# Kernel optimization log

Hardware: AMD Instinct MI355X
Metric: run time of the kernel (lower is better)

Reference implementation:

```python
import jax, jax.numpy as jnp
import numpy as np

B, D, C, K = 1024, 64, 100000, 5  # batch, feature dim, n_classes, positives per sample


def setup_inputs() -> dict:
    key = jax.random.key(0)
    k1, k2, k3 = jax.random.split(key, 3)
    x = jax.random.normal(k1, (B, D), dtype=jnp.float32)
    W = jax.random.normal(k2, (D, C), dtype=jnp.float32) * 0.02
    b = jnp.zeros((C,), dtype=jnp.float32)
    # K distinct positive class ids per sample (setdiff1d assume_unique requires distinct)
    base = jax.random.randint(k3, (B, 1), 0, C)
    labels = (base + jnp.arange(K, dtype=jnp.int64)[None, :]) % C
    return {"x": x, "labels": labels, "W": W, "b": b}


def reference(x, labels, W, b):
    # classifier: logits [B, C]
    logits = x @ W + b
    # Original loop: for each positive p of a sample, CE over [p] + negatives
    # (negatives = all classes except ALL positives of that sample), label 0:
    #   loss_p = -(l_p - log(exp(l_p) + sum_{c in negatives} exp(l_c)))
    # Vectorized via total expsum minus the positives' contribution.
    m = jnp.max(logits, axis=1, keepdims=True)                    # [B, 1]
    e = jnp.exp(logits - m)                                       # [B, C]
    total = jnp.sum(e, axis=1, keepdims=True)                     # [B, 1]
    pos_logits = jnp.take_along_axis(logits, labels, axis=1)      # [B, K]
    pos_e = jnp.exp(pos_logits - m)                               # [B, K]
    neg_sum = total - jnp.sum(pos_e, axis=1, keepdims=True)       # [B, 1]
    denom = pos_e + neg_sum                                       # [B, K]
    losses = -(pos_logits - m - jnp.log(denom))                   # [B, K]
    # sum over all (sample, positive) pairs / total number of positives
    return jnp.sum(losses) / losses.size
```

## Files before the change

### kernel.cpp

```cpp
#include <hip/hip_runtime.h>

constexpr int Bn = 1024;
constexpr int Dn = 64;
constexpr int Cn = 100000;
constexpr int Kn = 5;
constexpr float LOG2E = 1.44269504088896f;
constexpr float LN2   = 0.69314718055994531f;

typedef float f32x4  __attribute__((ext_vector_type(4)));
typedef short bf16x8 __attribute__((ext_vector_type(8)));

__device__ __forceinline__ unsigned short f32_to_bf16(float f) {
  union { float f; unsigned int u; } v; v.f = f;
  unsigned int r = v.u + 0x7FFFu + ((v.u >> 16) & 1u);
  return (unsigned short)(r >> 16);
}
__device__ __forceinline__ float bf16_to_f32(unsigned short u) {
  union { unsigned int i; float f; } v; v.i = ((unsigned int)u) << 16; return v.f;
}

constexpr int SPLITS = 125;
constexpr int CPS    = Cn / SPLITS;
constexpr int NCH    = CPS / 32;
constexpr int GRID   = SPLITS * 4;
constexpr int NBLK_W = (Cn + 63) / 64;

__global__ __launch_bounds__(256) void prep_kernel(
    const float* __restrict__ x, const float* __restrict__ W,
    unsigned short* __restrict__ xb, unsigned short* __restrict__ Wt,
    float* __restrict__ out)
{
  const int tid = threadIdx.x;
  const int b   = blockIdx.x;
  if (b == 0 && tid == 0) *out = 0.f;
  if (b < NBLK_W) {
    __shared__ unsigned short tile[64][71];
    const int c0   = b * 64;
    const int cIdx = tid & 63, dIdx = tid >> 6;
#pragma unroll
    for (int k = 0; k < 16; ++k) {
      const int d = dIdx * 16 + k;
      const int c = c0 + cIdx;
      const float v = (c < Cn) ? W[(size_t)d * Cn + c] : 0.f;
      tile[d][cIdx] = f32_to_bf16(v);
    }
    __syncthreads();
    const int cl = tid >> 2, dq = tid & 3;
    if (c0 + cl < Cn) {
      bf16x8 o0, o1;
#pragma unroll
      for (int k = 0; k < 8; ++k) o0[k] = (short)tile[dq * 16 + k][cl];
#pragma unroll
      for (int k = 0; k < 8; ++k) o1[k] = (short)tile[dq * 16 + 8 + k][cl];
      unsigned short* dst = Wt + (size_t)(c0 + cl) * 64 + dq * 16;
      *reinterpret_cast<bf16x8*>(dst)     = o0;
      *reinterpret_cast<bf16x8*>(dst + 8) = o1;
    }
  } else {
    const int i = ((b - NBLK_W) * 256 + tid) * 4;
    if (i < Bn * Dn) {
      const float4 v = *reinterpret_cast<const float4*>(x + i);
      ushort4 o;
      o.x = f32_to_bf16(v.x * LOG2E); o.y = f32_to_bf16(v.y * LOG2E);
      o.z = f32_to_bf16(v.z * LOG2E); o.w = f32_to_bf16(v.w * LOG2E);
      *reinterpret_cast<ushort4*>(xb + i) = o;
    }
  }
}

__device__ __forceinline__ void loadChunk(
    const unsigned short* __restrict__ Wt, const float* __restrict__ bias,
    int cb, int lr, int lg, bf16x8 (&b)[2][2], float (&bb)[2])
{
  const unsigned short* p0 = Wt + (size_t)(cb + lr) * 64 + lg * 8;
  const unsigned short* p1 = p0 + 16 * 64;
  b[0][0] = *reinterpret_cast<const bf16x8*>(p0);
  b[0][1] = *reinterpret_cast<const bf16x8*>(p0 + 32);
  b[1][0] = *reinterpret_cast<const bf16x8*>(p1);
  b[1][1] = *reinterpret_cast<const bf16x8*>(p1 + 32);
  bb[0] = bias[cb + lr] * LOG2E;
  bb[1] = bias[cb + 16 + lr] * LOG2E;
}

__device__ __forceinline__ void computeChunk(
    const bf16x8 (&a)[4][2], const bf16x8 (&b)[2][2], const float (&bb)[2],
    float (&esum)[4][4])
{
  f32x4 acc[4][2];
#pragma unroll
  for (int t = 0; t < 4; ++t) {
    acc[t][0] = f32x4{bb[0], bb[0], bb[0], bb[0]};
    acc[t][1] = f32x4{bb[1], bb[1], bb[1], bb[1]};
  }
#pragma unroll
  for (int t = 0; t < 4; ++t) {
    acc[t][0] = __builtin_amdgcn_mfma_f32_16x16x32_bf16(a[t][0], b[0][0], acc[t][0], 0, 0, 0);
    acc[t][1] = __builtin_amdgcn_mfma_f32_16x16x32_bf16(a[t][0], b[1][0], acc[t][1], 0, 0, 0);
    acc[t][0] = __builtin_amdgcn_mfma_f32_16x16x32_bf16(a[t][1], b[0][1], acc[t][0], 0, 0, 0);
    acc[t][1] = __builtin_amdgcn_mfma_f32_16x16x32_bf16(a[t][1], b[1][1], acc[t][1], 0, 0, 0);
  }
#pragma unroll
  for (int t = 0; t < 4; ++t)
#pragma unroll
    for (int j = 0; j < 4; ++j) {
      const float e0 = __builtin_amdgcn_exp2f(acc[t][0][j]);
      const float e1 = __builtin_amdgcn_exp2f(acc[t][1][j]);
      esum[t][j] += e0 + e1;
    }
}

__global__ __launch_bounds__(256) void gemm_expsum_kernel(
    const unsigned short* __restrict__ xb, const unsigned short* __restrict__ Wt,
    const float* __restrict__ bias, float* __restrict__ P)
{
  const int b   = blockIdx.x;
  const int xcd = b & 7, bs = b >> 3;
  const int wgid = (xcd < 4 ? xcd * 63 : 252 + (xcd - 4) * 62) + bs;
  const int split = wgid >> 2, sgrp = wgid & 3;

  const int tid  = threadIdx.x;
  const int lane = tid & 63, wid = tid >> 6;
  const int lr = lane & 15, lg = lane >> 4;
  const int sbase = sgrp * 256 + wid * 64;
  const int cb0   = split * CPS;

  bf16x8 a[4][2];
#pragma unroll
  for (int t = 0; t < 4; ++t) {
    const unsigned short* ap = xb + (size_t)(sbase + t * 16 + lr) * 64 + lg * 8;
    a[t][0] = *reinterpret_cast<const bf16x8*>(ap);
    a[t][1] = *reinterpret_cast<const bf16x8*>(ap + 32);
  }

  float esum[4][4];
#pragma unroll
  for (int t = 0; t < 4; ++t)
#pragma unroll
    for (int j = 0; j < 4; ++j) esum[t][j] = 0.f;

  bf16x8 bX[2][2]; float bbX[2];
  bf16x8 bY[2][2]; float bbY[2];
  loadChunk(Wt, bias, cb0, lr, lg, bX, bbX);
#pragma unroll 1
  for (int ch = 0; ch < NCH; ch += 2) {
    if (ch + 1 < NCH) loadChunk(Wt, bias, cb0 + (ch + 1) * 32, lr, lg, bY, bbY);
    computeChunk(a, bX, bbX, esum);
    if (ch + 1 < NCH) {
      if (ch + 2 < NCH) loadChunk(Wt, bias, cb0 + (ch + 2) * 32, lr, lg, bX, bbX);
      computeChunk(a, bY, bbY, esum);
    }
  }

  float red[4][4];
#pragma unroll
  for (int t = 0; t < 4; ++t)
#pragma unroll
    for (int j = 0; j < 4; ++j) {
      float v = esum[t][j];
      v += __shfl_xor(v, 1, 64);
      v += __shfl_xor(v, 2, 64);
      v += __shfl_xor(v, 4, 64);
      v += __shfl_xor(v, 8, 64);
      red[t][j] = v;
    }
  if (lr == 0) {
#pragma unroll
    for (int t = 0; t < 4; ++t)
#pragma unroll
      for (int j = 0; j < 4; ++j)
        P[(size_t)(sbase + t * 16 + lg * 4 + j) * SPLITS + split] = red[t][j];
  }
}

__global__ __launch_bounds__(64) void loss2_kernel(
    const unsigned short* __restrict__ xb, const int* __restrict__ labels,
    const unsigned short* __restrict__ Wt, const float* __restrict__ bias,
    const float* __restrict__ P, float* __restrict__ out)
{
  const int i = blockIdx.x, lane = threadIdx.x;
  float acc = P[(size_t)i * SPLITS + lane];
  if (lane + 64 < SPLITS) acc += P[(size_t)i * SPLITS + lane + 64];
#pragma unroll
  for (int off = 32; off > 0; off >>= 1) acc += __shfl_xor(acc, off, 64);
  const float Si = acc;

  const float xv = bf16_to_f32(xb[i * Dn + lane]);
  float l2[Kn];
#pragma unroll
  for (int p = 0; p < Kn; ++p) {
    const int c = labels[i * Kn + p];
    float v = xv * bf16_to_f32(Wt[(size_t)c * 64 + lane]);
#pragma unroll
    for (int off = 32; off > 0; off >>= 1) v += __shfl_xor(v, off, 64);
    l2[p] = v + bias[c] * LOG2E;
  }
  if (lane == 0) {
    float Psum = 0.f;
#pragma unroll
    for (int p = 0; p < Kn; ++p) Psum += __builtin_amdgcn_exp2f(l2[p]);
    const float neg = Si - Psum;
    float lsum = 0.f;
#pragma unroll
    for (int p = 0; p < Kn; ++p)
      lsum += __logf(__builtin_amdgcn_exp2f(l2[p]) + neg) - l2[p] * LN2;
    atomicAdd(out, lsum * (1.0f / (float)(Bn * Kn)));
  }
}

constexpr int NB  = 128;
constexpr int NPB = (Cn + NB - 1) / NB;
constexpr int NPBpad = 784;

__global__ __launch_bounds__(256) void cvt_x_kernel(
    const float* __restrict__ x, unsigned short* __restrict__ xb)
{
  const int i = (blockIdx.x * 256 + threadIdx.x) * 4;
  const float4 v = *reinterpret_cast<const float4*>(x + i);
  ushort4 o;
  o.x = f32_to_bf16(v.x); o.y = f32_to_bf16(v.y);
  o.z = f32_to_bf16(v.z); o.w = f32_to_bf16(v.w);
  *reinterpret_cast<ushort4*>(xb + i) = o;
}

__global__ __launch_bounds__(256) void expsum_mfma_kernel(
    const unsigned short* __restrict__ xb, const float* __restrict__ W,
    const float* __restrict__ bias, float* __restrict__ P,
    float* __restrict__ S, int use_partials)
{
  __shared__ float S_lds[4][Bn];
  const int tid  = threadIdx.x;
  const int lane = tid & 63, wid = tid >> 6;
  const int lg = lane >> 4, lr = lane & 15;
  const int cbase = blockIdx.x * NB + wid * 32;

  for (int i = tid; i < 4 * Bn; i += 256) (&S_lds[0][0])[i] = 0.f;

  bf16x8 bfrag[2][2];
  float  bval[2];
#pragma unroll
  for (int t = 0; t < 2; ++t) {
    const int c  = cbase + t * 16 + lr;
    const bool ok = (c < Cn);
    bval[t] = ok ? bias[c] * LOG2E : -1e38f;
#pragma unroll
    for (int h = 0; h < 2; ++h) {
      bf16x8 bf;
#pragma unroll
      for (int j = 0; j < 8; ++j) {
        const int d = h * 32 + lg * 8 + j;
        const float w = ok ? W[(size_t)d * Cn + c] : 0.f;
        bf[j] = (short)f32_to_bf16(w);
      }
      bfrag[t][h] = bf;
    }
  }
  __syncthreads();

#pragma unroll 1
  for (int ch = 0; ch < Bn / 16; ++ch) {
    const int s = ch * 16 + lr;
    const bf16x8 a0 = *reinterpret_cast<const bf16x8*>(xb + (size_t)s * Dn + lg * 8);
    const bf16x8 a1 = *reinterpret_cast<const bf16x8*>(xb + (size_t)s * Dn + 32 + lg * 8);
    f32x4 acc0 = {0.f, 0.f, 0.f, 0.f};
    f32x4 acc1 = {0.f, 0.f, 0.f, 0.f};
    acc0 = __builtin_amdgcn_mfma_f32_16x16x32_bf16(a0, bfrag[0][0], acc0, 0, 0, 0);
    acc1 = __builtin_amdgcn_mfma_f32_16x16x32_bf16(a0, bfrag[1][0], acc1, 0, 0, 0);
    acc0 = __builtin_amdgcn_mfma_f32_16x16x32_bf16(a1, bfrag[0][1], acc0, 0, 0, 0);
    acc1 = __builtin_amdgcn_mfma_f32_16x16x32_bf16(a1, bfrag[1][1], acc1, 0, 0, 0);

    float v[4];
#pragma unroll
    for (int j = 0; j < 4; ++j) {
      const float e0 = __builtin_amdgcn_exp2f(fmaf(acc0[j], LOG2E, bval[0]));
      const float e1 = __builtin_amdgcn_exp2f(fmaf(acc1[j], LOG2E, bval[1]));
      v[j] = e0 + e1;
    }
#pragma unroll
    for (int j = 0; j < 4; ++j) {
      v[j] += __shfl_xor(v[j], 1, 64);
      v[j] += __shfl_xor(v[j], 2, 64);
      v[j] += __shfl_xor(v[j], 4, 64);
      v[j] += __shfl_xor(v[j], 8, 64);
    }
    if (lr == 0) {
#pragma unroll
      for (int j = 0; j < 4; ++j)
        S_lds[wid][ch * 16 + lg * 4 + j] += v[j];
    }
  }
  __syncthreads();

  if (use_partials) {
    for (int s2 = tid; s2 < Bn; s2 += 256) {
      const float v = S_lds[0][s2] + S_lds[1][s2] + S_lds[2][s2] + S_lds[3][s2];
      P[(size_t)s2 * NPBpad + blockIdx.x] = v;
    }
  } else {
    for (int s2 = tid; s2 < Bn; s2 += 256) {
      const float v = S_lds[0][s2] + S_lds[1][s2] + S_lds[2][s2] + S_lds[3][s2];
      atomicAdd(&S[s2], v);
    }
  }
}

__global__ __launch_bounds__(64) void loss_kernel(
    const float* __restrict__ x, const int* __restrict__ labels,
    const float* __restrict__ W, const float* __restrict__ bias,
    const float* __restrict__ P, const float* __restrict__ S,
    float* __restrict__ out, int use_partials)
{
  const int i    = blockIdx.x;
  const int lane = threadIdx.x;

  float Si;
  if (use_partials) {
    float acc = 0.f;
    for (int j = lane; j < NPB; j += 64) acc += P[(size_t)i * NPBpad + j];
#pragma unroll
    for (int off = 32; off > 0; off >>= 1) acc += __shfl_xor(acc, off, 64);
    Si = acc;
  } else {
    Si = S[i];
  }

  const float xv = x[i * Dn + lane];
  float l[Kn];
#pragma unroll
  for (int p = 0; p < Kn; ++p) {
    const int c = labels[i * Kn + p];
    float v = xv * W[(size_t)lane * Cn + c];
#pragma unroll
    for (int off = 32; off > 0; off >>= 1) v += __shfl_xor(v, off, 64);
    l[p] = v + bias[c];
  }

  if (lane == 0) {
    float Psum = 0.f;
#pragma unroll
    for (int p = 0; p < Kn; ++p) Psum += __expf(l[p]);
    const float neg = Si - Psum;
    float lsum = 0.f;
#pragma unroll
    for (int p = 0; p < Kn; ++p)
      lsum += __logf(__expf(l[p]) + neg) - l[p];
    atomicAdd(out, lsum * (1.0f / (float)(Bn * Kn)));
  }
}

extern "C" void kernel_launch(void* const* d_in, const int* in_sizes, int n_in,
                              void* d_out, int out_size, void* d_ws, size_t ws_size,
                              hipStream_t stream) {
  const float* x      = (const float*)d_in[0];
  const int*   labels = (const int*)d_in[1];
  const float* W      = (const float*)d_in[2];
  const float* bias   = (const float*)d_in[3];
  float*       out    = (float*)d_out;
  char*        ws     = (char*)d_ws;

  const size_t off_xb = 0;
  const size_t off_P  = (size_t)Bn * Dn * 2;
  const size_t off_Wt = off_P + (size_t)SPLITS * Bn * 4;
  const size_t need_new = off_Wt + (size_t)Cn * Dn * 2;

  if (ws_size >= need_new) {
    unsigned short* xb = (unsigned short*)(ws + off_xb);
    float*          P  = (float*)(ws + off_P);
    unsigned short* Wt = (unsigned short*)(ws + off_Wt);
    const int prep_blocks = NBLK_W + (Bn * Dn) / (256 * 4);
    prep_kernel<<<prep_blocks, 256, 0, stream>>>(x, W, xb, Wt, out);
    gemm_expsum_kernel<<<GRID, 256, 0, stream>>>(xb, Wt, bias, P);
    loss2_kernel<<<Bn, 64, 0, stream>>>(xb, labels, Wt, bias, P, out);
    return;
  }

  hipMemsetAsync(out, 0, sizeof(float), stream);
  float*          Sg = (float*)ws;
  unsigned short* xb = (unsigned short*)(ws + 4096);
  float*          Pp = (float*)(ws + 4096 + (size_t)Bn * Dn * 2);
  const size_t need_old = 4096 + (size_t)Bn * Dn * 2 + (size_t)Bn * NPBpad * 4;
  const int use_partials = (ws_size >= need_old) ? 1 : 0;
  if (!use_partials) hipMemsetAsync(Sg, 0, Bn * sizeof(float), stream);

  cvt_x_kernel<<<(Bn * Dn) / (256 * 4), 256, 0, stream>>>(x, xb);
  expsum_mfma_kernel<<<NPB, 256, 0, stream>>>(xb, W, bias, Pp, Sg, use_partials);
  loss_kernel<<<Bn, 64, 0, stream>>>(x, labels, W, bias, Pp, Sg, out, use_partials);
}
```

Measured before the change: 64.62 us.

## Split batch across more workgroups with one 16-row tile per wave

Measured after the change: 137.8 us. +113.2%, slower.

```diff
diff --git a/kernel.cpp b/kernel.cpp
--- a/kernel.cpp
+++ b/kernel.cpp
@@ -22,7 +22,8 @@
 constexpr int SPLITS = 125;
 constexpr int CPS    = Cn / SPLITS;
 constexpr int NCH    = CPS / 32;
-constexpr int GRID   = SPLITS * 4;
+constexpr int SGRPS  = 16;
+constexpr int GRID   = SPLITS * SGRPS;
 constexpr int NBLK_W = (Cn + 63) / 64;
 
 __global__ __launch_bounds__(256) void prep_kernel(
@@ -83,30 +84,21 @@
 }
 
 __device__ __forceinline__ void computeChunk(
-    const bf16x8 (&a)[4][2], const bf16x8 (&b)[2][2], const float (&bb)[2],
-    float (&esum)[4][4])
-{
-  f32x4 acc[4][2];
-#pragma unroll
-  for (int t = 0; t < 4; ++t) {
-    acc[t][0] = f32x4{bb[0], bb[0], bb[0], bb[0]};
-    acc[t][1] = f32x4{bb[1], bb[1], bb[1], bb[1]};
-  }
-#pragma unroll
-  for (int t = 0; t < 4; ++t) {
-    acc[t][0] = __builtin_amdgcn_mfma_f32_16x16x32_bf16(a[t][0], b[0][0], acc[t][0], 0, 0, 0);
-    acc[t][1] = __builtin_amdgcn_mfma_f32_16x16x32_bf16(a[t][0], b[1][0], acc[t][1], 0, 0, 0);
-    acc[t][0] = __builtin_amdgcn_mfma_f32_16x16x32_bf16(a[t][1], b[0][1], acc[t][0], 0, 0, 0);
-    acc[t][1] = __builtin_amdgcn_mfma_f32_16x16x32_bf16(a[t][1], b[1][1], acc[t][1], 0, 0, 0);
-  }
-#pragma unroll
-  for (int t = 0; t < 4; ++t)
-#pragma unroll
-    for (int j = 0; j < 4; ++j) {
-      const float e0 = __builtin_amdgcn_exp2f(acc[t][0][j]);
-      const float e1 = __builtin_amdgcn_exp2f(acc[t][1][j]);
-      esum[t][j] += e0 + e1;
-    }
+    const bf16x8 a0, const bf16x8 a1, const bf16x8 (&b)[2][2],
+    const float (&bb)[2], float (&esum)[4])
+{
+  f32x4 acc0 = {bb[0], bb[0], bb[0], bb[0]};
+  f32x4 acc1 = {bb[1], bb[1], bb[1], bb[1]};
+  acc0 = __builtin_amdgcn_mfma_f32_16x16x32_bf16(a0, b[0][0], acc0, 0, 0, 0);
+  acc1 = __builtin_amdgcn_mfma_f32_16x16x32_bf16(a0, b[1][0], acc1, 0, 0, 0);
+  acc0 = __builtin_amdgcn_mfma_f32_16x16x32_bf16(a1, b[0][1], acc0, 0, 0, 0);
+  acc1 = __builtin_amdgcn_mfma_f32_16x16x32_bf16(a1, b[1][1], acc1, 0, 0, 0);
+#pragma unroll
+  for (int j = 0; j < 4; ++j) {
+    const float e0 = __builtin_amdgcn_exp2f(acc0[j]);
+    const float e1 = __builtin_amdgcn_exp2f(acc1[j]);
+    esum[j] += e0 + e1;
+  }
 }
 
 __global__ __launch_bounds__(256) void gemm_expsum_kernel(
@@ -115,28 +107,22 @@
 {
   const int b   = blockIdx.x;
   const int xcd = b & 7, bs = b >> 3;
-  const int wgid = (xcd < 4 ? xcd * 63 : 252 + (xcd - 4) * 62) + bs;
-  const int split = wgid >> 2, sgrp = wgid & 3;
+  const int wgid  = xcd * 250 + bs;
+  const int split = wgid >> 4, sgrp = wgid & 15;
 
   const int tid  = threadIdx.x;
   const int lane = tid & 63, wid = tid >> 6;
   const int lr = lane & 15, lg = lane >> 4;
-  const int sbase = sgrp * 256 + wid * 64;
+  const int sbase = sgrp * 64 + wid * 16;
   const int cb0   = split * CPS;
 
-  bf16x8 a[4][2];
-#pragma unroll
-  for (int t = 0; t < 4; ++t) {
-    const unsigned short* ap = xb + (size_t)(sbase + t * 16 + lr) * 64 + lg * 8;
-    a[t][0] = *reinterpret_cast<const bf16x8*>(ap);
-    a[t][1] = *reinterpret_cast<const bf16x8*>(ap + 32);
-  }
-
-  float esum[4][4];
-#pragma unroll
-  for (int t = 0; t < 4; ++t)
-#pragma unroll
-    for (int j = 0; j < 4; ++j) esum[t][j] = 0.f;
+  const unsigned short* ap = xb + (size_t)(sbase + lr) * 64 + lg * 8;
+  const bf16x8 a0 = *reinterpret_cast<const bf16x8*>(ap);
+  const bf16x8 a1 = *reinterpret_cast<const bf16x8*>(ap + 32);
+
+  float esum[4];
+#pragma unroll
+  for (int j = 0; j < 4; ++j) esum[j] = 0.f;
 
   bf16x8 bX[2][2]; float bbX[2];
   bf16x8 bY[2][2]; float bbY[2];
@@ -144,31 +130,27 @@
 #pragma unroll 1
   for (int ch = 0; ch < NCH; ch += 2) {
     if (ch + 1 < NCH) loadChunk(Wt, bias, cb0 + (ch + 1) * 32, lr, lg, bY, bbY);
-    computeChunk(a, bX, bbX, esum);
+    computeChunk(a0, a1, bX, bbX, esum);
     if (ch + 1 < NCH) {
       if (ch + 2 < NCH) loadChunk(Wt, bias, cb0 + (ch + 2) * 32, lr, lg, bX, bbX);
-      computeChunk(a, bY, bbY, esum);
-    }
-  }
-
-  float red[4][4];
-#pragma unroll
-  for (int t = 0; t < 4; ++t)
-#pragma unroll
-    for (int j = 0; j < 4; ++j) {
-      float v = esum[t][j];
-      v += __shfl_xor(v, 1, 64);
-      v += __shfl_xor(v, 2, 64);
-      v += __shfl_xor(v, 4, 64);
-      v += __shfl_xor(v, 8, 64);
-      red[t][j] = v;
-    }
+      computeChunk(a0, a1, bY, bbY, esum);
+    }
+  }
+
+  float red[4];
+#pragma unroll
+  for (int j = 0; j < 4; ++j) {
+    float v = esum[j];
+    v += __shfl_xor(v, 1, 64);
+    v += __shfl_xor(v, 2, 64);
+    v += __shfl_xor(v, 4, 64);
+    v += __shfl_xor(v, 8, 64);
+    red[j] = v;
+  }
   if (lr == 0) {
 #pragma unroll
-    for (int t = 0; t < 4; ++t)
-#pragma unroll
-      for (int j = 0; j < 4; ++j)
-        P[(size_t)(sbase + t * 16 + lg * 4 + j) * SPLITS + split] = red[t][j];
+    for (int j = 0; j < 4; ++j)
+      P[(size_t)(sbase + lg * 4 + j) * SPLITS + split] = red[j];
   }
 }
 
```
